# Kernel optimization log

Measured on AMD Instinct MI355X. Metric: run time of the kernel, lower is better.

## Reference

```python
import jax, jax.numpy as jnp
import numpy as np
import math

jax.config.update("jax_enable_x64", True)

# cfg constants
N = 4096
DIM = 16
SA = 2.0        # sigma_a
SR = 0.5        # sigma_r
V_SCALE = 1.0
R_H = 6.0
TAU_H = 0.5
K0_KUR = 0.05
TAU_KUR = 2.0
EPS = 1e-7      # acosh clamp epsilon (K=1 curvature)
D_MIN = 0.08    # distance floor in pairwise_dist


def setup_inputs() -> dict:
    key = jax.random.key(0)
    d_star = SA * SR / (SA - SR) * math.log(SA / SR)
    r_init = 0.5 * d_star
    hs = jax.random.normal(key, (N, DIM), dtype=jnp.float64) * r_init
    ht = jnp.sqrt(1.0 + jnp.sum(hs ** 2, axis=-1, keepdims=True))
    h = jnp.concatenate([ht, hs], axis=-1)  # [N, DIM+1] on the hyperboloid
    return {"h": h}


def reference(h):
    """Pairwise hyperbolic distance -> LJ coupling K_geo -> Lorentz-log force F,
    plus LJ potential energy E. Matmul form: no [N,N,dim+1] intermediates."""
    n1 = h.shape[-1]
    metric = jnp.concatenate([-jnp.ones((1,), h.dtype), jnp.ones((n1 - 1,), h.dtype)])
    # Lorentz inner products for all pairs: [N, N] (fp64)
    inn = (h * metric) @ h.T
    # geodesic distance d = acosh(clamp(-<hi,hj>_L, 1+eps))  (K = 1)
    D = jnp.arccosh(jnp.clip(-inn, 1.0 + EPS))
    eye = jnp.eye(N, dtype=h.dtype)
    # exact pairwise_dist semantics: zero diag, add D_MIN to off-diag entries < D_MIN
    D_pair = D * (1.0 - eye) + D_MIN * (((D < D_MIN) & (eye < 0.5)).astype(h.dtype))

    # _build_K in float32 (K_local == 1 since use_dyn_curv=False, learn_K=False)
    D_f = D_pair.astype(jnp.float32)
    eye32 = eye.astype(jnp.float32)
    D_eff = jnp.clip(D_f, 0.05)  # (D / sqrt(clamp(Ki*Kj,1e-4))).clamp(min=0.05) with K_local=1
    dVdd = jnp.exp(-D_eff / SR) / SR - jnp.exp(-D_eff / SA) / SA
    K_geo = -dVdd * V_SCALE * (1.0 - eye32)
    K_geo = K_geo * jax.nn.sigmoid((R_H - D_eff) / TAU_H)  # causal horizon
    K_kur = K0_KUR * jnp.exp(-D_f / TAU_KUR) * (1.0 - eye32)

    # _force: F_i = sum_j K_geo_ij * log_{h_i}(h_j)
    # log_x(y) = d / sqrt(<x,y>^2 - 1) * (y + <x,y> x)
    denom = jnp.sqrt(jnp.clip(inn ** 2 - 1.0, 1e-15))
    C = K_geo.astype(h.dtype) * D / denom  # [N, N]; diag is 0 since K_geo diag is 0
    F = C @ h + jnp.sum(C * inn, axis=-1, keepdims=True) * h  # [N, DIM+1]
    F_norm = jnp.clip(jnp.linalg.norm(F, axis=-1, keepdims=True), 1e-8)
    F = F * jnp.minimum(6.0 / F_norm, 1.0)

    # lj_potential energy on D_pair
    V = V_SCALE * (jnp.exp(-D_pair / SA) - jnp.exp(-D_pair / SR))
    E = jnp.sum(V * (1.0 - eye)) * 0.5
    return F, E
```

## Files before the change

kernel.cpp:

```cpp
#include <hip/hip_runtime.h>

#define NPTS 4096
#define DIMP 17
#define ROWP 20
#define RROW 21
#define JPB  128
#define NSLAB (NPTS / JPB)
#define NIB   (NPTS / 64)
#define EOFF  (NSLAB * NPTS * ROWP)
#define NEP   (NIB * NSLAB)
#define REDF  (192 * RROW)
#define MAXOFF 278460u

typedef float v4f  __attribute__((ext_vector_type(4)));
typedef float v16f __attribute__((ext_vector_type(16)));

#define SWAIT() do {                                        \
    asm volatile("s_waitcnt lgkmcnt(0)" ::: "memory");      \
    __builtin_amdgcn_sched_barrier(0);                      \
} while (0)

#define SLOAD(B, B16, OFF) do {                                         \
    const char* _p = hb + (OFF);                                        \
    asm volatile("s_load_dwordx16 %0, %1, 0x0"                          \
                 : "=&s"(B) : "s"(_p));                                 \
    asm volatile("s_load_dword %0, %1, 0x40"                            \
                 : "=&s"(B16) : "s"(_p));                               \
} while (0)

#define PAIR(B, B16) do {                                               \
    float p0 = nh[0] * (B)[0], p1 = nh[1] * (B)[1];                     \
    p0 = fmaf(nh[2],  (B)[2],  p0);  p1 = fmaf(nh[3],  (B)[3],  p1);    \
    p0 = fmaf(nh[4],  (B)[4],  p0);  p1 = fmaf(nh[5],  (B)[5],  p1);    \
    p0 = fmaf(nh[6],  (B)[6],  p0);  p1 = fmaf(nh[7],  (B)[7],  p1);    \
    p0 = fmaf(nh[8],  (B)[8],  p0);  p1 = fmaf(nh[9],  (B)[9],  p1);    \
    p0 = fmaf(nh[10], (B)[10], p0);  p1 = fmaf(nh[11], (B)[11], p1);    \
    p0 = fmaf(nh[12], (B)[12], p0);  p1 = fmaf(nh[13], (B)[13], p1);    \
    p0 = fmaf(nh[14], (B)[14], p0);  p1 = fmaf(nh[15], (B)[15], p1);    \
    const float m  = fmaf(nh[16], (B16), p0 + p1);         \
    const float ss = fmaxf(fmaf(m, m, -1.0f), 2e-7f);       \
    const float r  = __builtin_amdgcn_rsqf(ss);             \
    const float sq = ss * r;                                  \
    const float w  = ((m - 1.0f) - sq) + 1.0f;              \
    const float d  = -__logf(w);                                        \
    const float t  = __builtin_amdgcn_sqrtf(w);           \
    const float u  = w * w;                                \
    const float sg = u * __builtin_amdgcn_rcpf(u + 6.1442123533e-6f);   \
    const float K  = fmaf(0.5f, t, -2.0f * u) * sg;                     \
    const float C  = K * d * r;                                         \
    eacc += (t - u);                                                    \
    sm = fmaf(C, m, sm);                                                \
    ac[0]  = fmaf(C, (B)[0],  ac[0]);  ac[1]  = fmaf(C, (B)[1],  ac[1]);\
    ac[2]  = fmaf(C, (B)[2],  ac[2]);  ac[3]  = fmaf(C, (B)[3],  ac[3]);\
    ac[4]  = fmaf(C, (B)[4],  ac[4]);  ac[5]  = fmaf(C, (B)[5],  ac[5]);\
    ac[6]  = fmaf(C, (B)[6],  ac[6]);  ac[7]  = fmaf(C, (B)[7],  ac[7]);\
    ac[8]  = fmaf(C, (B)[8],  ac[8]);  ac[9]  = fmaf(C, (B)[9],  ac[9]);\
    ac[10] = fmaf(C, (B)[10], ac[10]); ac[11] = fmaf(C, (B)[11], ac[11]);\
    ac[12] = fmaf(C, (B)[12], ac[12]); ac[13] = fmaf(C, (B)[13], ac[13]);\
    ac[14] = fmaf(C, (B)[14], ac[14]); ac[15] = fmaf(C, (B)[15], ac[15]);\
    ac[16] = fmaf(C, (B16), ac[16]);                                    \
} while (0)

__global__ __launch_bounds__(256) void hydra_pair_kernel(
    const float* __restrict__ h, float* __restrict__ ws,
    float* __restrict__ out, const int use_ws) {
    const int tid  = threadIdx.x;
    const int lane = tid & 63;
    const int wid  = tid >> 6;
    const int i    = blockIdx.x * 64 + lane;

    __shared__ float lds[REDF + 16];

    float nh[DIMP];
#pragma unroll
    for (int k = 0; k < DIMP; ++k) nh[k] = -h[i * DIMP + k];
    nh[0] = -nh[0];

    float ac[DIMP];
#pragma unroll
    for (int k = 0; k < DIMP; ++k) ac[k] = 0.0f;
    float sm = 0.0f, eacc = 0.0f;

    const char* hb = (const char*)h;
    const unsigned base_off = (unsigned)__builtin_amdgcn_readfirstlane(
        (int)((blockIdx.y * JPB + wid * 32) * (DIMP * 4)));

    v16f bA, bB; float tA, tB;
    SLOAD(bA, tA, base_off);
    for (int jj = 0; jj < 32; jj += 2) {
        unsigned o1 = base_off + (unsigned)(jj + 1) * 68u;
        unsigned o2 = base_off + (unsigned)(jj + 2) * 68u;
        if (o2 > MAXOFF) o2 = MAXOFF;
        SWAIT();
        SLOAD(bB, tB, o1);
        PAIR(bA, tA);
        SWAIT();
        SLOAD(bA, tA, o2);
        PAIR(bB, tB);
    }

    ac[0] = fmaf(-sm, nh[0], ac[0]);
#pragma unroll
    for (int k = 1; k < DIMP; ++k) ac[k] = fmaf(sm, nh[k], ac[k]);

#pragma unroll
    for (int off = 32; off > 0; off >>= 1) eacc += __shfl_xor(eacc, off);

    __syncthreads();
    if (wid > 0) {
        float* dst = lds + ((wid - 1) * 64 + lane) * RROW;
#pragma unroll
        for (int k = 0; k < DIMP; ++k) dst[k] = ac[k];
        if (lane == 0) lds[REDF + wid] = eacc;
    }
    __syncthreads();

    if (wid == 0) {
        const float esum = eacc + lds[REDF + 1] + lds[REDF + 2] + lds[REDF + 3];
#pragma unroll
        for (int q = 0; q < 3; ++q) {
            const float* src = lds + (q * 64 + lane) * RROW;
#pragma unroll
            for (int k = 0; k < DIMP; ++k) ac[k] += src[k];
        }
        if (use_ws) {
            float* dst = ws + ((size_t)blockIdx.y * NPTS + i) * ROWP;
#pragma unroll
            for (int k = 0; k < DIMP; ++k) dst[k] = ac[k];
            if (lane == 0) ws[EOFF + blockIdx.y * NIB + blockIdx.x] = esum;
        } else {
#pragma unroll
            for (int k = 0; k < DIMP; ++k) atomicAdd(&out[i * DIMP + k], ac[k]);
            if (lane == 0) atomicAdd(&out[NPTS * DIMP], esum);
        }
    }
}

__global__ __launch_bounds__(256) void hydra_finalize_kernel(
    const float* __restrict__ ws, float* __restrict__ out, const int use_ws) {
    const int tid  = threadIdx.x;
    const int lane = tid & 63;
    const int q    = tid >> 6;
    const int i    = blockIdx.x * 64 + lane;

    __shared__ __align__(16) float red[3 * 64 * RROW + 8];

    float v[DIMP];
#pragma unroll
    for (int k = 0; k < DIMP; ++k) v[k] = 0.0f;

    if (use_ws) {
#pragma unroll
        for (int ssl = 0; ssl < NSLAB / 4; ++ssl) {
            const int s = q * (NSLAB / 4) + ssl;
            const float* row = ws + ((size_t)s * NPTS + i) * ROWP;
            const v4f b0 = ((const v4f*)row)[0];
            const v4f b1 = ((const v4f*)row)[1];
            const v4f b2 = ((const v4f*)row)[2];
            const v4f b3 = ((const v4f*)row)[3];
            v[0]  += b0.x; v[1]  += b0.y; v[2]  += b0.z; v[3]  += b0.w;
            v[4]  += b1.x; v[5]  += b1.y; v[6]  += b1.z; v[7]  += b1.w;
            v[8]  += b2.x; v[9]  += b2.y; v[10] += b2.z; v[11] += b2.w;
            v[12] += b3.x; v[13] += b3.y; v[14] += b3.z; v[15] += b3.w;
            v[16] += row[16];
        }
        if (q > 0) {
            float* dst = red + ((q - 1) * 64 + lane) * RROW;
#pragma unroll
            for (int k = 0; k < DIMP; ++k) dst[k] = v[k];
        }
        __syncthreads();
        if (q == 0) {
#pragma unroll
            for (int qq = 0; qq < 3; ++qq) {
                const float* src = red + (qq * 64 + lane) * RROW;
#pragma unroll
                for (int k = 0; k < DIMP; ++k) v[k] += src[k];
            }
        }
    } else if (q == 0) {
#pragma unroll
        for (int k = 0; k < DIMP; ++k) v[k] = out[i * DIMP + k];
    }

    if (q == 0) {
        float ss = 0.0f;
#pragma unroll
        for (int k = 0; k < DIMP; ++k) ss = fmaf(v[k], v[k], ss);
        const float nrm   = sqrtf(ss);
        const float scale = fminf(6.0f / fmaxf(nrm, 1e-8f), 1.0f);
#pragma unroll
        for (int k = 0; k < DIMP; ++k) out[i * DIMP + k] = v[k] * scale;
    }

    if (blockIdx.x == 0) {
        if (use_ws) {
            float e = 0.0f;
#pragma unroll
            for (int t = 0; t < NEP / 256; ++t) e += ws[EOFF + tid + t * 256];
#pragma unroll
            for (int off = 32; off > 0; off >>= 1) e += __shfl_xor(e, off);
            __shared__ float es[4];
            if (lane == 0) es[q] = e;
            __syncthreads();
            if (tid == 0) out[NPTS * DIMP] = 0.5f * (es[0] + es[1] + es[2] + es[3]);
        } else {
            if (tid == 0) out[NPTS * DIMP] *= 0.5f;
        }
    }
}

extern "C" void kernel_launch(void* const* d_in, const int* in_sizes, int n_in,
                              void* d_out, int out_size, void* d_ws, size_t ws_size,
                              hipStream_t stream) {
    const float* h = (const float*)d_in[0];
    float* out = (float*)d_out;
    float* ws  = (float*)d_ws;

    const size_t need = (size_t)(EOFF + NEP) * sizeof(float);
    const int use_ws = (ws_size >= need) ? 1 : 0;
    if (!use_ws) {
        hipMemsetAsync(d_out, 0, (size_t)out_size * sizeof(float), stream);
    }

    dim3 grid(NIB, NSLAB);
    hydra_pair_kernel<<<grid, 256, 0, stream>>>(h, ws, out, use_ws);
    hydra_finalize_kernel<<<64, 256, 0, stream>>>(ws, out, use_ws);
}
```

Before: 39.49 us.

## Use bf16 MFMA for inner products and force accumulation

Replaces the scalar-load, per-thread FMA pair loop with bf16 32x32x16 MFMA tiles. One MFMA computes the Lorentz inner products and a second accumulates C times h_j, with j-points staged transposed in swizzled LDS. The grid is reorganized into 32-row i-blocks by 512-column j-blocks, giving 32 slabs for the finalize pass. This cuts the VALU FMA work, but bf16 rounding of h and C risks accuracy in acosh near d≈0 and in the force sums.

```diff
diff --git a/kernel.cpp b/kernel.cpp
--- a/kernel.cpp
+++ b/kernel.cpp
@@ -4,135 +4,145 @@
 #define DIMP 17
 #define ROWP 20
 #define RROW 21
-#define JPB  128
-#define NSLAB (NPTS / JPB)
-#define NIB   (NPTS / 64)
-#define EOFF  (NSLAB * NPTS * ROWP)
-#define NEP   (NIB * NSLAB)
-#define REDF  (192 * RROW)
-#define MAXOFF 278460u
-
+#define FSLAB 32
+#define NIBT  128
+#define EOFF  (FSLAB * NPTS * ROWP)
+#define NEP   (FSLAB * NIBT)
+
+typedef short s8v  __attribute__((ext_vector_type(8)));
+typedef float f16v __attribute__((ext_vector_type(16)));
 typedef float v4f  __attribute__((ext_vector_type(4)));
-typedef float v16f __attribute__((ext_vector_type(16)));
-
-#define SWAIT() do {                                        \
-    asm volatile("s_waitcnt lgkmcnt(0)" ::: "memory");      \
-    __builtin_amdgcn_sched_barrier(0);                      \
-} while (0)
-
-#define SLOAD(B, B16, OFF) do {                                         \
-    const char* _p = hb + (OFF);                                        \
-    asm volatile("s_load_dwordx16 %0, %1, 0x0"                          \
-                 : "=&s"(B) : "s"(_p));                                 \
-    asm volatile("s_load_dword %0, %1, 0x40"                            \
-                 : "=&s"(B16) : "s"(_p));                               \
-} while (0)
-
-#define PAIR(B, B16) do {                                               \
-    float p0 = nh[0] * (B)[0], p1 = nh[1] * (B)[1];                     \
-    p0 = fmaf(nh[2],  (B)[2],  p0);  p1 = fmaf(nh[3],  (B)[3],  p1);    \
-    p0 = fmaf(nh[4],  (B)[4],  p0);  p1 = fmaf(nh[5],  (B)[5],  p1);    \
-    p0 = fmaf(nh[6],  (B)[6],  p0);  p1 = fmaf(nh[7],  (B)[7],  p1);    \
-    p0 = fmaf(nh[8],  (B)[8],  p0);  p1 = fmaf(nh[9],  (B)[9],  p1);    \
-    p0 = fmaf(nh[10], (B)[10], p0);  p1 = fmaf(nh[11], (B)[11], p1);    \
-    p0 = fmaf(nh[12], (B)[12], p0);  p1 = fmaf(nh[13], (B)[13], p1);    \
-    p0 = fmaf(nh[14], (B)[14], p0);  p1 = fmaf(nh[15], (B)[15], p1);    \
-    const float m  = fmaf(nh[16], (B16), p0 + p1);         \
-    const float ss = fmaxf(fmaf(m, m, -1.0f), 2e-7f);       \
-    const float r  = __builtin_amdgcn_rsqf(ss);             \
-    const float sq = ss * r;                                  \
-    const float w  = ((m - 1.0f) - sq) + 1.0f;              \
-    const float d  = -__logf(w);                                        \
-    const float t  = __builtin_amdgcn_sqrtf(w);           \
-    const float u  = w * w;                                \
-    const float sg = u * __builtin_amdgcn_rcpf(u + 6.1442123533e-6f);   \
-    const float K  = fmaf(0.5f, t, -2.0f * u) * sg;                     \
-    const float C  = K * d * r;                                         \
-    eacc += (t - u);                                                    \
-    sm = fmaf(C, m, sm);                                                \
-    ac[0]  = fmaf(C, (B)[0],  ac[0]);  ac[1]  = fmaf(C, (B)[1],  ac[1]);\
-    ac[2]  = fmaf(C, (B)[2],  ac[2]);  ac[3]  = fmaf(C, (B)[3],  ac[3]);\
-    ac[4]  = fmaf(C, (B)[4],  ac[4]);  ac[5]  = fmaf(C, (B)[5],  ac[5]);\
-    ac[6]  = fmaf(C, (B)[6],  ac[6]);  ac[7]  = fmaf(C, (B)[7],  ac[7]);\
-    ac[8]  = fmaf(C, (B)[8],  ac[8]);  ac[9]  = fmaf(C, (B)[9],  ac[9]);\
-    ac[10] = fmaf(C, (B)[10], ac[10]); ac[11] = fmaf(C, (B)[11], ac[11]);\
-    ac[12] = fmaf(C, (B)[12], ac[12]); ac[13] = fmaf(C, (B)[13], ac[13]);\
-    ac[14] = fmaf(C, (B)[14], ac[14]); ac[15] = fmaf(C, (B)[15], ac[15]);\
-    ac[16] = fmaf(C, (B16), ac[16]);                                    \
+
+__device__ __forceinline__ unsigned short f2bf(float x) {
+    union { float f; unsigned u; } v; v.f = x;
+    return (unsigned short)((v.u + 0x7FFFu + ((v.u >> 16) & 1u)) >> 16);
+}
+__device__ __forceinline__ unsigned pk2(float a, float b) {
+    return (unsigned)f2bf(a) | ((unsigned)f2bf(b) << 16);
+}
+
+#define XF(MV, CV) do {                                                  \
+    const float _m  = (MV);                                              \
+    const float _ss = fmaxf(fmaf(_m, _m, -1.0f), 2e-7f);     \
+    const float _r  = __builtin_amdgcn_rsqf(_ss);            \
+    const float _sq = _ss * _r;                               \
+    const float _w  = ((_m - 1.0f) - _sq) + 1.0f;             \
+    const float _d  = -__logf(_w);                                       \
+    const float _t  = __builtin_amdgcn_sqrtf(_w);            \
+    const float _u  = _w * _w;                                \
+    const float _sg = _u * __builtin_amdgcn_rcpf(_u + 6.1442123533e-6f); \
+    const float _K  = fmaf(0.5f, _t, -2.0f * _u) * _sg;                  \
+    (CV) = _K * _d * _r;                                                 \
+    eacc += (_t - _u);                                                   \
+    sm = fmaf((CV), _m, sm);                                             \
 } while (0)
 
 __global__ __launch_bounds__(256) void hydra_pair_kernel(
     const float* __restrict__ h, float* __restrict__ ws,
     float* __restrict__ out, const int use_ws) {
-    const int tid  = threadIdx.x;
-    const int lane = tid & 63;
-    const int wid  = tid >> 6;
-    const int i    = blockIdx.x * 64 + lane;
-
-    __shared__ float lds[REDF + 16];
-
-    float nh[DIMP];
-#pragma unroll
-    for (int k = 0; k < DIMP; ++k) nh[k] = -h[i * DIMP + k];
-    nh[0] = -nh[0];
-
-    float ac[DIMP];
-#pragma unroll
-    for (int k = 0; k < DIMP; ++k) ac[k] = 0.0f;
+    const int tid = threadIdx.x, lane = tid & 63, wid = tid >> 6;
+    const int hlf = lane >> 5, n = lane & 31;
+    const int ib = blockIdx.x * 32, jb = blockIdx.y * 512;
+
+    __shared__ __align__(16) char Tb[17 * 1024];
+    __shared__ float TI[17 * 33];
+    __shared__ float SA[4][32];
+
+    for (int t2 = tid; t2 < 17 * 256; t2 += 256) {
+        const int d = t2 >> 8, jp = (t2 & 255) * 2;
+        const float f0 = h[(jb + jp) * DIMP + d];
+        const float f1 = h[(jb + jp + 1) * DIMP + d];
+        *(unsigned*)(Tb + ((d * 1024 + jp * 2) ^ ((d & 7) << 4))) = pk2(f0, f1);
+    }
+    for (int t2 = tid; t2 < 17 * 32; t2 += 256) {
+        const int d = t2 >> 5, ii = t2 & 31;
+        TI[d * 33 + ii] = h[(ib + ii) * DIMP + d];
+    }
+
+    s8v bfr, b2 = (s8v)(short)0;
+    {
+        const int irow = ib + n;
+#pragma unroll
+        for (int e = 0; e < 8; ++e) {
+            const int k = 8 * hlf + e;
+            float v = h[irow * DIMP + k];
+            if (k != 0) v = -v;
+            bfr[e] = (short)f2bf(v);
+        }
+        if (hlf == 0) b2[0] = (short)f2bf(-h[irow * DIMP + 16]);
+    }
+    __syncthreads();
+
+    f16v facc = (f16v)(0.0f);
     float sm = 0.0f, eacc = 0.0f;
 
-    const char* hb = (const char*)h;
-    const unsigned base_off = (unsigned)__builtin_amdgcn_readfirstlane(
-        (int)((blockIdx.y * JPB + wid * 32) * (DIMP * 4)));
-
-    v16f bA, bB; float tA, tB;
-    SLOAD(bA, tA, base_off);
-    for (int jj = 0; jj < 32; jj += 2) {
-        unsigned o1 = base_off + (unsigned)(jj + 1) * 68u;
-        unsigned o2 = base_off + (unsigned)(jj + 2) * 68u;
-        if (o2 > MAXOFF) o2 = MAXOFF;
-        SWAIT();
-        SLOAD(bB, tB, o1);
-        PAIR(bA, tA);
-        SWAIT();
-        SLOAD(bA, tA, o2);
-        PAIR(bB, tB);
-    }
-
-    ac[0] = fmaf(-sm, nh[0], ac[0]);
-#pragma unroll
-    for (int k = 1; k < DIMP; ++k) ac[k] = fmaf(sm, nh[k], ac[k]);
-
+    for (int t = 0; t < 4; ++t) {
+        const int jt = wid * 4 + t;
+        const int jr = jb + jt * 32 + n;
+
+        s8v afr, a2 = (s8v)(short)0;
+#pragma unroll
+        for (int e = 0; e < 8; ++e)
+            afr[e] = (short)f2bf(h[jr * DIMP + 8 * hlf + e]);
+        if (hlf == 0) a2[0] = (short)f2bf(h[jr * DIMP + 16]);
+
+        f16v g = (f16v)(0.0f);
+        g = __builtin_amdgcn_mfma_f32_32x32x16_bf16(afr, bfr, g, 0, 0, 0);
+        g = __builtin_amdgcn_mfma_f32_32x32x16_bf16(a2, b2, g, 0, 0, 0);
+
+        unsigned w[8];
+#pragma unroll
+        for (int q = 0; q < 8; ++q) {
+            float C0, C1;
+            XF(g[2 * q], C0);
+            XF(g[2 * q + 1], C1);
+            w[q] = pk2(C0, C1);
+        }
+        unsigned o[8];
+#pragma unroll
+        for (int q = 0; q < 8; ++q) o[q] = (unsigned)__shfl_xor((int)w[q], 32);
+
+#pragma unroll
+        for (int c = 0; c < 2; ++c) {
+            union { unsigned u[4]; s8v s; } pa;
+            pa.u[0] = hlf ? o[4 * c + 2] : w[4 * c];
+            pa.u[1] = hlf ? o[4 * c + 3] : w[4 * c + 1];
+            pa.u[2] = hlf ? w[4 * c + 2] : o[4 * c];
+            pa.u[3] = hlf ? w[4 * c + 3] : o[4 * c + 1];
+            const int dimc = (n > 16) ? 16 : n;
+            const int joff = jt * 32 + c * 16 + hlf * 8;
+            s8v pb = *(const s8v*)(Tb + ((dimc * 1024 + joff * 2) ^ ((dimc & 7) << 4)));
+            if (n > 16) pb = (s8v)(short)0;
+            facc = __builtin_amdgcn_mfma_f32_32x32x16_bf16(pa.s, pb, facc, 0, 0, 0);
+        }
+    }
+
+    sm += __shfl_xor(sm, 32);
+    if (lane < 32) SA[wid][lane] = sm;
 #pragma unroll
     for (int off = 32; off > 0; off >>= 1) eacc += __shfl_xor(eacc, off);
 
-    __syncthreads();
-    if (wid > 0) {
-        float* dst = lds + ((wid - 1) * 64 + lane) * RROW;
-#pragma unroll
-        for (int k = 0; k < DIMP; ++k) dst[k] = ac[k];
-        if (lane == 0) lds[REDF + wid] = eacc;
-    }
-    __syncthreads();
-
-    if (wid == 0) {
-        const float esum = eacc + lds[REDF + 1] + lds[REDF + 2] + lds[REDF + 3];
-#pragma unroll
-        for (int q = 0; q < 3; ++q) {
-            const float* src = lds + (q * 64 + lane) * RROW;
-#pragma unroll
-            for (int k = 0; k < DIMP; ++k) ac[k] += src[k];
-        }
-        if (use_ws) {
-            float* dst = ws + ((size_t)blockIdx.y * NPTS + i) * ROWP;
-#pragma unroll
-            for (int k = 0; k < DIMP; ++k) dst[k] = ac[k];
-            if (lane == 0) ws[EOFF + blockIdx.y * NIB + blockIdx.x] = esum;
-        } else {
-#pragma unroll
-            for (int k = 0; k < DIMP; ++k) atomicAdd(&out[i * DIMP + k], ac[k]);
-            if (lane == 0) atomicAdd(&out[NPTS * DIMP], esum);
-        }
+    const int slab = blockIdx.y * 4 + wid;
+    if (use_ws) {
+        if (n < DIMP) {
+#pragma unroll
+            for (int r = 0; r < 16; ++r) {
+                const int irow = (r & 3) + 8 * (r >> 2) + 4 * hlf;
+                const float val = facc[r] - SA[wid][irow] * TI[n * 33 + irow];
+                ws[(size_t)(slab * NPTS + ib + irow) * ROWP + n] = val;
+            }
+        }
+        if (lane == 0) ws[EOFF + slab * NIBT + blockIdx.x] = eacc;
+    } else {
+        if (n < DIMP) {
+#pragma unroll
+            for (int r = 0; r < 16; ++r) {
+                const int irow = (r & 3) + 8 * (r >> 2) + 4 * hlf;
+                atomicAdd(&out[(ib + irow) * DIMP + n],
+                          facc[r] - SA[wid][irow] * TI[n * 33 + irow]);
+            }
+        }
+        if (lane == 0) atomicAdd(&out[NPTS * DIMP], eacc);
     }
 }
 
@@ -151,8 +161,8 @@
 
     if (use_ws) {
 #pragma unroll
-        for (int ssl = 0; ssl < NSLAB / 4; ++ssl) {
-            const int s = q * (NSLAB / 4) + ssl;
+        for (int ssl = 0; ssl < FSLAB / 4; ++ssl) {
+            const int s = q * (FSLAB / 4) + ssl;
             const float* row = ws + ((size_t)s * NPTS + i) * ROWP;
             const v4f b0 = ((const v4f*)row)[0];
             const v4f b1 = ((const v4f*)row)[1];
@@ -223,7 +233,7 @@
         hipMemsetAsync(d_out, 0, (size_t)out_size * sizeof(float), stream);
     }
 
-    dim3 grid(NIB, NSLAB);
+    dim3 grid(NIBT, 8);
     hydra_pair_kernel<<<grid, 256, 0, stream>>>(h, ws, out, use_ws);
     hydra_finalize_kernel<<<64, 256, 0, stream>>>(ws, out, use_ws);
 }
```

Measured after the change: 49.31 us. 24.9% more time.
